# Kernel optimization log

Hardware: AMD Instinct MI355X
Metric: run time of the kernel (lower is better)

The kernel has to match this reference:

```python
import jax, jax.numpy as jnp
import numpy as np

B, T, E, H, K, V = 256, 200, 100, 128, 13, 50000


def run_lstm(x, W, U, b, reverse=False):
    """Keras LSTM with activation=relu, recurrent_activation=sigmoid.
    x: [B,T,E]; W: [E,4H]; U: [H,4H]; b: [4H]. Gate order: i, f, g, o.
    Returns hidden states [B,T,H] (time-aligned for both directions)."""
    Bn = x.shape[0]
    Hn = U.shape[0]
    xw = jnp.einsum('bte,eg->btg', x, W) + b  # precompute input projections [B,T,4H]

    def step(carry, xw_t):
        h, c = carry
        z = xw_t + h @ U
        i, f, g, o = jnp.split(z, 4, axis=-1)
        i = jax.nn.sigmoid(i)
        f = jax.nn.sigmoid(f)
        g = jax.nn.relu(g)          # activation=relu (non-cuDNN path in TF)
        c = f * c + i * g
        h = o * jax.nn.relu(c)      # output activation also relu
        return (h, c), h

    init = (jnp.zeros((Bn, Hn), x.dtype), jnp.zeros((Bn, Hn), x.dtype))
    _, hs = jax.lax.scan(step, init, jnp.swapaxes(xw, 0, 1), reverse=reverse)
    return jnp.swapaxes(hs, 0, 1)


def crf_log_likelihood(logits, labels, lens, trans):
    """tfa.text.crf_log_likelihood: score(labels) - logZ, masked by seq lens."""
    Bn, Tn, Kn = logits.shape
    t_idx = jnp.arange(Tn)
    mask = t_idx[None, :] < lens[:, None]  # [B,T]
    # unary score
    unary = jnp.take_along_axis(logits, labels[..., None], axis=-1)[..., 0]
    u_score = jnp.sum(jnp.where(mask, unary, 0.0), axis=-1)
    # transition score
    pair = trans[labels[:, :-1], labels[:, 1:]]  # [B,T-1]
    pmask = t_idx[None, 1:] < lens[:, None]
    b_score = jnp.sum(jnp.where(pmask, pair, 0.0), axis=-1)
    # forward algorithm (log-space DP over time, masked updates)
    def step(alpha, inp):
        logit_t, valid = inp  # [B,K], [B]
        new = jax.nn.logsumexp(alpha[:, :, None] + trans[None], axis=1) + logit_t
        alpha = jnp.where(valid[:, None], new, alpha)
        return alpha, None

    alpha0 = logits[:, 0, :]
    xs = (jnp.swapaxes(logits[:, 1:, :], 0, 1), jnp.swapaxes(mask[:, 1:], 0, 1))
    alpha, _ = jax.lax.scan(step, alpha0, xs)
    logZ = jax.nn.logsumexp(alpha, axis=-1)
    return u_score + b_score - logZ


def setup_inputs() -> dict:
    key = jax.random.key(0)
    ks = jax.random.split(key, 12)
    s = lambda k, shape, sc: jax.random.normal(k, shape, jnp.float32) * sc
    return {
        'text': jax.random.randint(ks[0], (B, T), 0, V).astype(jnp.int32),
        'labels': jax.random.randint(ks[1], (B, T), 0, K).astype(jnp.int32),
        'emb': s(ks[2], (V, E), 0.1),
        'Wf': s(ks[3], (E, 4 * H), 0.05),
        'Uf': s(ks[4], (H, 4 * H), 0.05),
        'bf': jnp.zeros((4 * H,), jnp.float32),
        'Wb': s(ks[5], (E, 4 * H), 0.05),
        'Ub': s(ks[6], (H, 4 * H), 0.05),
        'bb': jnp.zeros((4 * H,), jnp.float32),
        'Wd': s(ks[7], (2 * H, K), 0.05),
        'bd': jnp.zeros((K,), jnp.float32),
        'trans': jax.random.uniform(ks[8], (K, K), jnp.float32),
    }


def reference(text, labels, emb, Wf, Uf, bf, Wb, Ub, bb, Wd, bd, trans):
    lens = jnp.sum((text != 0).astype(jnp.int32), axis=-1)  # [B]
    x = emb[text]                      # embedding lookup [B,T,E]
    # dropout is identity in eval mode
    h_fwd = run_lstm(x, Wf, Uf, bf, reverse=False)
    h_bwd = run_lstm(x, Wb, Ub, bb, reverse=True)
    h = jnp.concatenate([h_fwd, h_bwd], axis=-1)  # [B,T,2H]
    logits = jax.nn.softmax(h @ Wd + bd, axis=-1)  # Dense(softmax), per source
    log_likelihood = crf_log_likelihood(logits, labels, lens, trans)
    return logits, lens, log_likelihood
```

## Files before the change

kernel.cpp:

```cpp
#include <hip/hip_runtime.h>
#include <hip/hip_bf16.h>

#define Bn 256
#define Tn 200
#define En 100
#define Hn 128
#define Kn 13
#define G4 512
#define BT 51200

typedef __attribute__((ext_vector_type(8))) __bf16 bf8_t;
typedef __attribute__((ext_vector_type(4))) unsigned short us4_t;
typedef __attribute__((ext_vector_type(4))) float f4_t;

__device__ __forceinline__ unsigned short f2bf(float f) {
  unsigned int u = __float_as_uint(f);
  u = (u + 0x7FFFu + ((u >> 16) & 1u)) >> 16;
  return (unsigned short)u;
}
__device__ __forceinline__ float bf2f(unsigned short s) {
  return __uint_as_float(((unsigned int)s) << 16);
}
__device__ __forceinline__ float sigm(float x) { return 1.f / (1.f + __expf(-x)); }

__device__ __forceinline__ void bar_lgkm() {
  asm volatile("s_waitcnt lgkmcnt(0)" ::: "memory");
  __builtin_amdgcn_s_barrier();
  __builtin_amdgcn_sched_barrier(0);
}

__device__ __forceinline__ int gperm(int n) {
  return ((n >> 4) & 3) * 128 + ((n >> 6) << 4) + (n & 15);
}

__global__ __launch_bounds__(64) void k_lens(const int* __restrict__ text,
                                             int* __restrict__ lens_i,
                                             float* __restrict__ out_lens) {
  int b = blockIdx.x, lane = threadIdx.x;
  int cnt = 0;
  for (int t = lane; t < Tn; t += 64) cnt += (text[b * Tn + t] != 0);
  for (int off = 32; off; off >>= 1) cnt += __shfl_down(cnt, off);
  if (lane == 0) { lens_i[b] = cnt; out_lens[b] = (float)cnt; }
}

__global__ __launch_bounds__(256) void k_wt(const float* __restrict__ Wf,
                                            const float* __restrict__ Wb,
                                            const float* __restrict__ Uf,
                                            const float* __restrict__ Ub,
                                            unsigned short* __restrict__ wt,
                                            unsigned short* __restrict__ ut) {
  int idx = blockIdx.x * 256 + threadIdx.x;
  int half = idx >> 17;
  int rem = idx & 131071;
  int dir = rem >> 16;
  int nk = rem & 65535;
  int n = nk >> 7, k = nk & 127;
  int mc = gperm(n);
  if (half == 0) {
    const float* W = dir ? Wb : Wf;
    wt[rem] = f2bf((k < En) ? W[k * G4 + mc] : 0.f);
  } else {
    const float* U = dir ? Ub : Uf;
    ut[rem] = f2bf(U[k * G4 + mc]);
  }
}

__global__ __launch_bounds__(256) void k_gather(const int* __restrict__ text,
                                                const float* __restrict__ emb,
                                                unsigned short* __restrict__ xg) {
  int row = blockIdx.x * 128 + (threadIdx.x >> 1);
  int half = threadIdx.x & 1;
  int tok = text[row];
  const float* er = emb + (size_t)tok * En;
  unsigned short* xr = xg + (size_t)row * 128 + half * 64;
  #pragma unroll
  for (int c = 0; c < 64; c += 2) {
    int col = half * 64 + c;
    float v0 = (col < En) ? er[col] : 0.f;
    float v1 = (col + 1 < En) ? er[col + 1] : 0.f;
    unsigned int pk = (unsigned int)f2bf(v0) | ((unsigned int)f2bf(v1) << 16);
    *(unsigned int*)(xr + c) = pk;
  }
}

__global__ __launch_bounds__(256) void k_gemm_xw(const unsigned short* __restrict__ xg,
                                                 const unsigned short* __restrict__ wt,
                                                 const float* __restrict__ biasf,
                                                 const float* __restrict__ biasb,
                                                 unsigned short* __restrict__ xwf,
                                                 unsigned short* __restrict__ xwb) {
  __shared__ unsigned short As[128 * 128];
  __shared__ unsigned short Bs[128 * 128];
  int mt = blockIdx.x;
  int dir = blockIdx.y >> 2;
  int nt = blockIdx.y & 3;
  const float* bias = dir ? biasb : biasf;
  unsigned short* out = dir ? xwb : xwf;
  int tid = threadIdx.x;
  const unsigned short* wt_d = wt + (size_t)dir * (G4 * 128);

  #pragma unroll
  for (int it = 0; it < 8; it++) {
    int idx = it * 256 + tid;
    int r = idx >> 4, c = idx & 15;
    bf8_t va = *(const bf8_t*)(xg + ((size_t)mt * 128 + r) * 128 + c * 8);
    bf8_t vb = *(const bf8_t*)(wt_d + ((size_t)nt * 128 + r) * 128 + c * 8);
    int byte = (r * 256 + c * 16) ^ ((r & 7) << 4);
    *(bf8_t*)((char*)As + byte) = va;
    *(bf8_t*)((char*)Bs + byte) = vb;
  }
  __syncthreads();
  int wid = tid >> 6, lane = tid & 63;
  int wm = wid >> 1, wn = wid & 1;
  int lr = lane & 15, lk = lane >> 4;
  f4_t zero = {0.f, 0.f, 0.f, 0.f};
  f4_t acc[4][4];
  #pragma unroll
  for (int m = 0; m < 4; m++)
    #pragma unroll
    for (int n = 0; n < 4; n++) acc[m][n] = zero;
  #pragma unroll
  for (int kk = 0; kk < 4; kk++) {
    bf8_t af[4], bv[4];
    #pragma unroll
    for (int m = 0; m < 4; m++) {
      int r = wm * 64 + m * 16 + lr;
      int byte = (r * 256 + kk * 64 + lk * 16) ^ ((r & 7) << 4);
      af[m] = *(const bf8_t*)((const char*)As + byte);
    }
    #pragma unroll
    for (int n = 0; n < 4; n++) {
      int r = wn * 64 + n * 16 + lr;
      int byte = (r * 256 + kk * 64 + lk * 16) ^ ((r & 7) << 4);
      bv[n] = *(const bf8_t*)((const char*)Bs + byte);
    }
    #pragma unroll
    for (int m = 0; m < 4; m++)
      #pragma unroll
      for (int n = 0; n < 4; n++)
        acc[m][n] = __builtin_amdgcn_mfma_f32_16x16x32_bf16(af[m], bv[n], acc[m][n], 0, 0, 0);
  }
  float bn[4];
  #pragma unroll
  for (int n = 0; n < 4; n++) {
    int colg = nt * 128 + wn * 64 + n * 16 + lr;
    bn[n] = bias[gperm(colg)];
  }
  int w2 = nt * 2 + wn;
  #pragma unroll
  for (int m = 0; m < 4; m++) {
    int rowl = wm * 64 + m * 16 + lk * 4;
    #pragma unroll
    for (int q = 0; q < 4; q++) {
      int row = mt * 128 + rowl + q;
      int b = row / 200;
      int t = row - b * 200;
      int bg = b >> 2, lg2 = b & 3;
      int tid2 = w2 * 64 + lg2 * 16 + lr;
      size_t dst = (((size_t)t * 64 + bg) * 512 + tid2) * 4;
      us4_t v;
      v[0] = f2bf(acc[m][0][q] + bn[0]);
      v[1] = f2bf(acc[m][1][q] + bn[1]);
      v[2] = f2bf(acc[m][2][q] + bn[2]);
      v[3] = f2bf(acc[m][3][q] + bn[3]);
      *(us4_t*)(out + dst) = v;
    }
  }
}

#define UB16(M) M(0,0) M(0,1) M(0,2) M(0,3) M(1,0) M(1,1) M(1,2) M(1,3) \
                M(2,0) M(2,1) M(2,2) M(2,3) M(3,0) M(3,1) M(3,2) M(3,3)

__global__ __attribute__((amdgpu_flat_work_group_size(512, 512),
                          amdgpu_waves_per_eu(1, 2)))
void k_scan(const unsigned short* __restrict__ ut,
            const unsigned short* __restrict__ xw2,
            unsigned short* __restrict__ hf,
            unsigned short* __restrict__ hb) {
  int blk = blockIdx.x;
  int dir = blk >> 6;
  int bg = blk & 63;
  int b0 = bg * 4;
  int tid = threadIdx.x;
  int w = tid >> 6, l = tid & 63;
  int lr = l & 15, lg = l >> 4;
  int jj = w * 16 + lr;
  const unsigned short* ut_d = ut + (size_t)dir * (G4 * 128);
  const unsigned short* xw_d = xw2 + (size_t)dir * ((size_t)BT * G4);
  unsigned short* hout = dir ? hb : hf;
  int t0 = dir ? (Tn - 1) : 0;
  int dt = dir ? -1 : 1;

#define LOADUB(nt, kk) \
  bf8_t ub_##nt##_##kk = *(const bf8_t*)(ut_d + (size_t)(w * 64 + (nt) * 16 + lr) * 128 + (kk) * 32 + lg * 8); \
  asm volatile("" : "+a"(ub_##nt##_##kk));
  UB16(LOADUB)
#undef LOADUB

  __shared__ unsigned short h_lds[2][2048];
  for (int i = tid; i < 2048; i += 512) ((unsigned int*)h_lds)[i] = 0;

  int rb0 = (lr * 256 +   0 + lg * 16) ^ ((lr & 7) << 4);
  int rb1 = (lr * 256 +  64 + lg * 16) ^ ((lr & 7) << 4);
  int rb2 = (lr * 256 + 128 + lg * 16) ^ ((lr & 7) << 4);
  int rb3 = (lr * 256 + 192 + lg * 16) ^ ((lr & 7) << 4);
  int wb = (((lg * 4) * 256 + jj * 2) ^ (((lg * 4) & 7) << 4)) + 4096;
  char* lbase = (char*)h_lds;

  const unsigned short* xptr = xw_d + (((size_t)t0 * 64 + bg) * 512 + tid) * 4;
  const long long xstep = (long long)dt * 131072;
  unsigned short* hp = hout + ((size_t)t0 * Bn + b0 + lg) * 128 + jj;
  const long long hstep = (long long)dt * Bn * 128;

  us4_t xa = *(const us4_t*)(xptr);
  us4_t xb = *(const us4_t*)(xptr + xstep);
  xptr += 2 * xstep;

  float c0 = 0.f;
  f4_t acc0 = {0.f,0.f,0.f,0.f}, acc1 = {0.f,0.f,0.f,0.f};
  f4_t acc2 = {0.f,0.f,0.f,0.f}, acc3 = {0.f,0.f,0.f,0.f};
  bar_lgkm();

#define MF(nt, kk) acc##nt = __builtin_amdgcn_mfma_f32_16x16x32_bf16(af##kk, ub_##nt##_##kk, acc##nt, 0, 0, 0);
#define STEP(X, ISSUE_OK) { \
    acc0[0] = bf2f(X[0]); acc1[0] = bf2f(X[1]); \
    acc2[0] = bf2f(X[2]); acc3[0] = bf2f(X[3]); \
    if (ISSUE_OK) { X = *(const us4_t*)(xptr); } \
    xptr += xstep; \
    bf8_t af0 = *(const bf8_t*)(lbase + rb0); \
    bf8_t af1 = *(const bf8_t*)(lbase + rb1); \
    bf8_t af2 = *(const bf8_t*)(lbase + rb2); \
    bf8_t af3 = *(const bf8_t*)(lbase + rb3); \
    MF(0,0) MF(1,0) MF(2,0) MF(3,0) \
    MF(0,1) MF(1,1) MF(2,1) MF(3,1) \
    MF(0,2) MF(1,2) MF(2,2) MF(3,2) \
    MF(0,3) MF(1,3) MF(2,3) MF(3,3) \
    float ig = sigm(acc0[0]); \
    float fg = sigm(acc1[0]); \
    float gg = fmaxf(acc2[0], 0.f); \
    c0 = fmaf(fg, c0, ig * gg); \
    unsigned short hs2 = f2bf(sigm(acc3[0]) * fmaxf(c0, 0.f)); \
    *(unsigned short*)(lbase + wb) = hs2; \
    bar_lgkm(); \
    hp[0] = hs2; \
    rb0 ^= 4096; rb1 ^= 4096; rb2 ^= 4096; rb3 ^= 4096; wb ^= 4096; \
    hp += hstep; }

  for (int tt = 0; tt < Tn; tt += 2) {
    STEP(xa, tt < Tn - 2)
    STEP(xb, tt < Tn - 3)
  }
#undef STEP
#undef MF
}

__global__ __launch_bounds__(128) void k_logits(const unsigned short* __restrict__ hf,
                                                const unsigned short* __restrict__ hb,
                                                const float* __restrict__ Wd,
                                                const float* __restrict__ bd,
                                                float* __restrict__ out) {
  __shared__ unsigned short hs[128 * 256];
  int tid = threadIdx.x;
  size_t row0 = (size_t)blockIdx.x * 128;
  #pragma unroll
  for (int it = 0; it < 16; it++) {
    int idx = it * 128 + tid;
    int r = idx >> 4, c = idx & 15;
    bf8_t vf = *(const bf8_t*)(hf + (row0 + r) * 128 + c * 8);
    bf8_t vb = *(const bf8_t*)(hb + (row0 + r) * 128 + c * 8);
    int byte = (r * 512 + c * 16) ^ ((r & 7) << 4);
    *(bf8_t*)((char*)hs + byte) = vf;
    int byte2 = (r * 512 + 256 + c * 16) ^ ((r & 7) << 4);
    *(bf8_t*)((char*)hs + byte2) = vb;
  }
  __syncthreads();
  float acc[Kn];
  #pragma unroll
  for (int jj = 0; jj < Kn; jj++) acc[jj] = bd[jj];
  int r = tid;
  #pragma unroll 4
  for (int c = 0; c < 32; c++) {
    int byte = (r * 512 + c * 16) ^ ((r & 7) << 4);
    bf8_t v = *(const bf8_t*)((const char*)hs + byte);
    #pragma unroll
    for (int e = 0; e < 8; e++) {
      float h = (float)v[e];
      int k = c * 8 + e;
      #pragma unroll
      for (int jj = 0; jj < Kn; jj++)
        acc[jj] = fmaf(h, Wd[k * Kn + jj], acc[jj]);
    }
  }
  float m = acc[0];
  #pragma unroll
  for (int jj = 1; jj < Kn; jj++) m = fmaxf(m, acc[jj]);
  float s = 0.f;
  #pragma unroll
  for (int jj = 0; jj < Kn; jj++) { acc[jj] = __expf(acc[jj] - m); s += acc[jj]; }
  float inv = 1.f / s;
  int rg = (int)row0 + tid;
  int b = rg & 255, t = rg >> 8;
  float* op = out + ((size_t)b * Tn + t) * Kn;
  #pragma unroll
  for (int jj = 0; jj < Kn; jj++) op[jj] = acc[jj] * inv;
}

__global__ __launch_bounds__(64) void k_crf(const float* __restrict__ logits,
                                            const int* __restrict__ labels,
                                            const int* __restrict__ lens_i,
                                            const float* __restrict__ trans,
                                            float* __restrict__ out_ll) {
  int b = blockIdx.x, lane = threadIdx.x;
  int len = lens_i[b];
  const float* lg = logits + (size_t)b * Tn * Kn;
  const int* lab = labels + (size_t)b * Tn;
  float sc = 0.f;
  for (int t = lane; t < Tn; t += 64) {
    if (t < len) {
      sc += lg[t * Kn + lab[t]];
      if (t >= 1) sc += trans[lab[t - 1] * Kn + lab[t]];
    }
  }
  for (int off = 32; off; off >>= 1) sc += __shfl_down(sc, off);
  bool act = lane < Kn;
  int jl = act ? lane : 0;
  float etr[Kn];
  #pragma unroll
  for (int i = 0; i < Kn; i++) etr[i] = __expf(trans[i * Kn + jl]);
  float a = act ? lg[jl] : -INFINITY;
  float lgv = (len > 1) ? lg[Kn + jl] : 0.f;
  for (int t = 1; t < len; t++) {
    float lgn = (t + 1 < len) ? lg[(t + 1) * Kn + jl] : 0.f;
    float m = a;
    for (int off = 8; off; off >>= 1) m = fmaxf(m, __shfl_xor(m, off, 16));
    float ea = __expf(a - m);
    float s = 0.f;
    #pragma unroll
    for (int i = 0; i < Kn; i++) s = fmaf(__shfl(ea, i), etr[i], s);
    float anew = m + __logf(s) + lgv;
    if (act) a = anew;
    lgv = lgn;
  }
  float m2 = a;
  for (int off = 8; off; off >>= 1) m2 = fmaxf(m2, __shfl_xor(m2, off, 16));
  float ea2 = act ? __expf(a - m2) : 0.f;
  float ssum = ea2;
  for (int off = 8; off; off >>= 1) ssum += __shfl_xor(ssum, off, 16);
  float logZ = m2 + __logf(ssum);
  if (lane == 0) out_ll[b] = sc - logZ;
}

extern "C" void kernel_launch(void* const* d_in, const int* in_sizes, int n_in,
                              void* d_out, int out_size, void* d_ws, size_t ws_size,
                              hipStream_t stream) {
  const int* text = (const int*)d_in[0];
  const int* labels = (const int*)d_in[1];
  const float* emb = (const float*)d_in[2];
  const float* Wf = (const float*)d_in[3];
  const float* Uf = (const float*)d_in[4];
  const float* bf_ = (const float*)d_in[5];
  const float* Wb = (const float*)d_in[6];
  const float* Ub = (const float*)d_in[7];
  const float* bb_ = (const float*)d_in[8];
  const float* Wd = (const float*)d_in[9];
  const float* bd = (const float*)d_in[10];
  const float* trans = (const float*)d_in[11];
  (void)in_sizes; (void)n_in; (void)out_size; (void)ws_size;

  float* out = (float*)d_out;
  float* out_logits = out;
  float* out_lens = out + (size_t)BT * Kn;
  float* out_ll = out_lens + Bn;

  char* ws = (char*)d_ws;
  size_t o = 0;
  int* lens_i = (int*)(ws + o);                o += 1024;
  unsigned short* wt = (unsigned short*)(ws + o);  o += (size_t)2 * G4 * 128 * 2;
  unsigned short* ut = (unsigned short*)(ws + o);  o += (size_t)2 * G4 * 128 * 2;
  unsigned short* xg = (unsigned short*)(ws + o);  o += (size_t)BT * 128 * 2;
  unsigned short* xw_s = (unsigned short*)(ws + o); o += (size_t)2 * BT * G4 * 2;
  unsigned short* hfb = (unsigned short*)(ws + o); o += (size_t)BT * Hn * 2;
  unsigned short* hbb = (unsigned short*)(ws + o); o += (size_t)BT * Hn * 2;
  unsigned short* xwf = xw_s;
  unsigned short* xwb = xw_s + (size_t)BT * G4;

  hipLaunchKernelGGL(k_lens, dim3(Bn), dim3(64), 0, stream, text, lens_i, out_lens);
  hipLaunchKernelGGL(k_wt, dim3(1024), dim3(256), 0, stream, Wf, Wb, Uf, Ub, wt, ut);
  hipLaunchKernelGGL(k_gather, dim3(400), dim3(256), 0, stream, text, emb, xg);
  hipLaunchKernelGGL(k_gemm_xw, dim3(400, 8), dim3(256), 0, stream, xg, wt, bf_, bb_, xwf, xwb);
  hipLaunchKernelGGL(k_scan, dim3(128), dim3(512), 0, stream, ut, xw_s, hfb, hbb);
  hipLaunchKernelGGL(k_logits, dim3(400), dim3(128), 0, stream, hfb, hbb, Wd, bd, out_logits);
  hipLaunchKernelGGL(k_crf, dim3(Bn), dim3(64), 0, stream, out_logits, labels, lens_i, trans, out_ll);
}
```

Measured before the change: 297.7 us.

## Fuse embedding gather into input GEMM and merge small prep kernels

Folds the embedding gather into the input-projection GEMM. Each 512-thread block now gathers 64 token rows straight into swizzled LDS, loads its slice of the weight matrix directly into registers, and covers all 512 gate columns. This removes the intermediate xg buffer and its round trip through memory. The lens and weight-transpose kernels become a single k_prep launch, which cuts launch overhead. The scan loop now issues its LDS loads before the x-projection prefetch and makes that prefetch unconditional. As a result it reads a little past the end of each direction's xw buffer, staying inside the workspace, in exchange for simpler scheduling.

```diff
diff --git a/kernel.cpp b/kernel.cpp
--- a/kernel.cpp
+++ b/kernel.cpp
@@ -33,130 +33,143 @@
   return ((n >> 4) & 3) * 128 + ((n >> 6) << 4) + (n & 15);
 }
 
-__global__ __launch_bounds__(64) void k_lens(const int* __restrict__ text,
-                                             int* __restrict__ lens_i,
-                                             float* __restrict__ out_lens) {
-  int b = blockIdx.x, lane = threadIdx.x;
-  int cnt = 0;
-  for (int t = lane; t < Tn; t += 64) cnt += (text[b * Tn + t] != 0);
-  for (int off = 32; off; off >>= 1) cnt += __shfl_down(cnt, off);
-  if (lane == 0) { lens_i[b] = cnt; out_lens[b] = (float)cnt; }
-}
-
-__global__ __launch_bounds__(256) void k_wt(const float* __restrict__ Wf,
-                                            const float* __restrict__ Wb,
-                                            const float* __restrict__ Uf,
-                                            const float* __restrict__ Ub,
-                                            unsigned short* __restrict__ wt,
-                                            unsigned short* __restrict__ ut) {
-  int idx = blockIdx.x * 256 + threadIdx.x;
-  int half = idx >> 17;
-  int rem = idx & 131071;
-  int dir = rem >> 16;
-  int nk = rem & 65535;
-  int n = nk >> 7, k = nk & 127;
-  int mc = gperm(n);
-  if (half == 0) {
-    const float* W = dir ? Wb : Wf;
-    wt[rem] = f2bf((k < En) ? W[k * G4 + mc] : 0.f);
+__global__ __launch_bounds__(256) void k_prep(const int* __restrict__ text,
+                                              const float* __restrict__ Wf,
+                                              const float* __restrict__ Wb,
+                                              const float* __restrict__ Uf,
+                                              const float* __restrict__ Ub,
+                                              unsigned short* __restrict__ wt,
+                                              unsigned short* __restrict__ ut,
+                                              int* __restrict__ lens_i,
+                                              float* __restrict__ out_lens) {
+  int bx = blockIdx.x;
+  if (bx < 1024) {
+    int idx = bx * 256 + threadIdx.x;
+    int half = idx >> 17;
+    int rem = idx & 131071;
+    int dir = rem >> 16;
+    int nk = rem & 65535;
+    int n = nk >> 7, k = nk & 127;
+    int mc = gperm(n);
+    if (half == 0) {
+      const float* W = dir ? Wb : Wf;
+      wt[rem] = f2bf((k < En) ? W[k * G4 + mc] : 0.f);
+    } else {
+      const float* U = dir ? Ub : Uf;
+      ut[rem] = f2bf(U[k * G4 + mc]);
+    }
   } else {
-    const float* U = dir ? Ub : Uf;
-    ut[rem] = f2bf(U[k * G4 + mc]);
-  }
-}
-
-__global__ __launch_bounds__(256) void k_gather(const int* __restrict__ text,
-                                                const float* __restrict__ emb,
-                                                unsigned short* __restrict__ xg) {
-  int row = blockIdx.x * 128 + (threadIdx.x >> 1);
-  int half = threadIdx.x & 1;
-  int tok = text[row];
-  const float* er = emb + (size_t)tok * En;
-  unsigned short* xr = xg + (size_t)row * 128 + half * 64;
-  #pragma unroll
-  for (int c = 0; c < 64; c += 2) {
-    int col = half * 64 + c;
-    float v0 = (col < En) ? er[col] : 0.f;
-    float v1 = (col + 1 < En) ? er[col + 1] : 0.f;
-    unsigned int pk = (unsigned int)f2bf(v0) | ((unsigned int)f2bf(v1) << 16);
-    *(unsigned int*)(xr + c) = pk;
-  }
-}
-
-__global__ __launch_bounds__(256) void k_gemm_xw(const unsigned short* __restrict__ xg,
+    int wi = threadIdx.x >> 6, lane = threadIdx.x & 63;
+    int b = (bx - 1024) * 4 + wi;
+    int cnt = 0;
+    for (int t = lane; t < Tn; t += 64) cnt += (text[b * Tn + t] != 0);
+    for (int off = 32; off; off >>= 1) cnt += __shfl_down(cnt, off);
+    if (lane == 0) { lens_i[b] = cnt; out_lens[b] = (float)cnt; }
+  }
+}
+
+#define NB16(M) M(0,0) M(0,1) M(0,2) M(0,3) M(1,0) M(1,1) M(1,2) M(1,3) \
+                M(2,0) M(2,1) M(2,2) M(2,3) M(3,0) M(3,1) M(3,2) M(3,3)
+
+__global__ __launch_bounds__(512) void k_gemm_xw(const int* __restrict__ text,
+                                                 const float* __restrict__ emb,
                                                  const unsigned short* __restrict__ wt,
                                                  const float* __restrict__ biasf,
                                                  const float* __restrict__ biasb,
                                                  unsigned short* __restrict__ xwf,
                                                  unsigned short* __restrict__ xwb) {
-  __shared__ unsigned short As[128 * 128];
-  __shared__ unsigned short Bs[128 * 128];
-  int mt = blockIdx.x;
-  int dir = blockIdx.y >> 2;
-  int nt = blockIdx.y & 3;
+  __shared__ unsigned short As[64 * 128];
+  int bx = blockIdx.x;
+  int dir = (bx >= 800);
+  int mt = dir ? bx - 800 : bx;
   const float* bias = dir ? biasb : biasf;
   unsigned short* out = dir ? xwb : xwf;
   int tid = threadIdx.x;
   const unsigned short* wt_d = wt + (size_t)dir * (G4 * 128);
 
-  #pragma unroll
-  for (int it = 0; it < 8; it++) {
-    int idx = it * 256 + tid;
-    int r = idx >> 4, c = idx & 15;
-    bf8_t va = *(const bf8_t*)(xg + ((size_t)mt * 128 + r) * 128 + c * 8);
-    bf8_t vb = *(const bf8_t*)(wt_d + ((size_t)nt * 128 + r) * 128 + c * 8);
-    int byte = (r * 256 + c * 16) ^ ((r & 7) << 4);
-    *(bf8_t*)((char*)As + byte) = va;
-    *(bf8_t*)((char*)Bs + byte) = vb;
-  }
+  {
+    int row = tid >> 3;
+    int oct = tid & 7;
+    int tok = text[mt * 64 + row];
+    const float* er = emb + (size_t)tok * En;
+    float fv[16];
+    #pragma unroll
+    for (int i = 0; i < 16; i++) fv[i] = 0.f;
+    if (oct < 6) {
+      #pragma unroll
+      for (int i = 0; i < 4; i++) {
+        float4 v = *(const float4*)(er + oct * 16 + i * 4);
+        fv[i * 4 + 0] = v.x; fv[i * 4 + 1] = v.y; fv[i * 4 + 2] = v.z; fv[i * 4 + 3] = v.w;
+      }
+    } else if (oct == 6) {
+      float4 v = *(const float4*)(er + 96);
+      fv[0] = v.x; fv[1] = v.y; fv[2] = v.z; fv[3] = v.w;
+    }
+    int swz = (row & 7) << 4;
+    #pragma unroll
+    for (int j = 0; j < 2; j++) {
+      unsigned short pk[8];
+      #pragma unroll
+      for (int e = 0; e < 8; e++) pk[e] = f2bf(fv[j * 8 + e]);
+      int byte = (row * 256 + oct * 32 + j * 16) ^ swz;
+      *(bf8_t*)((char*)As + byte) = *(bf8_t*)pk;
+    }
+  }
+
+  int w = tid >> 6, l = tid & 63;
+  int lr = l & 15, lg = l >> 4, lk = lg;
+#define LOADB(n, kk) \
+  bf8_t bb_##n##_##kk = *(const bf8_t*)(wt_d + (size_t)(w * 64 + (n) * 16 + lr) * 128 + (kk) * 32 + lg * 8);
+  NB16(LOADB)
+#undef LOADB
   __syncthreads();
-  int wid = tid >> 6, lane = tid & 63;
-  int wm = wid >> 1, wn = wid & 1;
-  int lr = lane & 15, lk = lane >> 4;
+
   f4_t zero = {0.f, 0.f, 0.f, 0.f};
   f4_t acc[4][4];
   #pragma unroll
   for (int m = 0; m < 4; m++)
     #pragma unroll
     for (int n = 0; n < 4; n++) acc[m][n] = zero;
-  #pragma unroll
-  for (int kk = 0; kk < 4; kk++) {
-    bf8_t af[4], bv[4];
-    #pragma unroll
-    for (int m = 0; m < 4; m++) {
-      int r = wm * 64 + m * 16 + lr;
-      int byte = (r * 256 + kk * 64 + lk * 16) ^ ((r & 7) << 4);
-      af[m] = *(const bf8_t*)((const char*)As + byte);
-    }
-    #pragma unroll
-    for (int n = 0; n < 4; n++) {
-      int r = wn * 64 + n * 16 + lr;
-      int byte = (r * 256 + kk * 64 + lk * 16) ^ ((r & 7) << 4);
-      bv[n] = *(const bf8_t*)((const char*)Bs + byte);
-    }
-    #pragma unroll
-    for (int m = 0; m < 4; m++)
-      #pragma unroll
-      for (int n = 0; n < 4; n++)
-        acc[m][n] = __builtin_amdgcn_mfma_f32_16x16x32_bf16(af[m], bv[n], acc[m][n], 0, 0, 0);
-  }
+
+  const char* lAs = (const char*)As;
+  int sz = (lr & 7) << 4;
+#define MFK(kk) { \
+    bf8_t a0 = *(const bf8_t*)(lAs + (((0 * 16 + lr) * 256 + (kk) * 64 + lg * 16) ^ sz)); \
+    bf8_t a1 = *(const bf8_t*)(lAs + (((1 * 16 + lr) * 256 + (kk) * 64 + lg * 16) ^ sz)); \
+    bf8_t a2 = *(const bf8_t*)(lAs + (((2 * 16 + lr) * 256 + (kk) * 64 + lg * 16) ^ sz)); \
+    bf8_t a3 = *(const bf8_t*)(lAs + (((3 * 16 + lr) * 256 + (kk) * 64 + lg * 16) ^ sz)); \
+    acc[0][0] = __builtin_amdgcn_mfma_f32_16x16x32_bf16(a0, bb_0_##kk, acc[0][0], 0, 0, 0); \
+    acc[0][1] = __builtin_amdgcn_mfma_f32_16x16x32_bf16(a0, bb_1_##kk, acc[0][1], 0, 0, 0); \
+    acc[0][2] = __builtin_amdgcn_mfma_f32_16x16x32_bf16(a0, bb_2_##kk, acc[0][2], 0, 0, 0); \
+    acc[0][3] = __builtin_amdgcn_mfma_f32_16x16x32_bf16(a0, bb_3_##kk, acc[0][3], 0, 0, 0); \
+    acc[1][0] = __builtin_amdgcn_mfma_f32_16x16x32_bf16(a1, bb_0_##kk, acc[1][0], 0, 0, 0); \
+    acc[1][1] = __builtin_amdgcn_mfma_f32_16x16x32_bf16(a1, bb_1_##kk, acc[1][1], 0, 0, 0); \
+    acc[1][2] = __builtin_amdgcn_mfma_f32_16x16x32_bf16(a1, bb_2_##kk, acc[1][2], 0, 0, 0); \
+    acc[1][3] = __builtin_amdgcn_mfma_f32_16x16x32_bf16(a1, bb_3_##kk, acc[1][3], 0, 0, 0); \
+    acc[2][0] = __builtin_amdgcn_mfma_f32_16x16x32_bf16(a2, bb_0_##kk, acc[2][0], 0, 0, 0); \
+    acc[2][1] = __builtin_amdgcn_mfma_f32_16x16x32_bf16(a2, bb_1_##kk, acc[2][1], 0, 0, 0); \
+    acc[2][2] = __builtin_amdgcn_mfma_f32_16x16x32_bf16(a2, bb_2_##kk, acc[2][2], 0, 0, 0); \
+    acc[2][3] = __builtin_amdgcn_mfma_f32_16x16x32_bf16(a2, bb_3_##kk, acc[2][3], 0, 0, 0); \
+    acc[3][0] = __builtin_amdgcn_mfma_f32_16x16x32_bf16(a3, bb_0_##kk, acc[3][0], 0, 0, 0); \
+    acc[3][1] = __builtin_amdgcn_mfma_f32_16x16x32_bf16(a3, bb_1_##kk, acc[3][1], 0, 0, 0); \
+    acc[3][2] = __builtin_amdgcn_mfma_f32_16x16x32_bf16(a3, bb_2_##kk, acc[3][2], 0, 0, 0); \
+    acc[3][3] = __builtin_amdgcn_mfma_f32_16x16x32_bf16(a3, bb_3_##kk, acc[3][3], 0, 0, 0); }
+  MFK(0) MFK(1) MFK(2) MFK(3)
+#undef MFK
+
   float bn[4];
   #pragma unroll
-  for (int n = 0; n < 4; n++) {
-    int colg = nt * 128 + wn * 64 + n * 16 + lr;
-    bn[n] = bias[gperm(colg)];
-  }
-  int w2 = nt * 2 + wn;
+  for (int n = 0; n < 4; n++) bn[n] = bias[gperm(w * 64 + n * 16 + lr)];
   #pragma unroll
   for (int m = 0; m < 4; m++) {
-    int rowl = wm * 64 + m * 16 + lk * 4;
+    int rowl = m * 16 + lk * 4;
     #pragma unroll
     for (int q = 0; q < 4; q++) {
-      int row = mt * 128 + rowl + q;
+      int row = mt * 64 + rowl + q;
       int b = row / 200;
       int t = row - b * 200;
       int bg = b >> 2, lg2 = b & 3;
-      int tid2 = w2 * 64 + lg2 * 16 + lr;
+      int tid2 = w * 64 + lg2 * 16 + lr;
       size_t dst = (((size_t)t * 64 + bg) * 512 + tid2) * 4;
       us4_t v;
       v[0] = f2bf(acc[m][0][q] + bn[0]);
@@ -222,15 +235,15 @@
   bar_lgkm();
 
 #define MF(nt, kk) acc##nt = __builtin_amdgcn_mfma_f32_16x16x32_bf16(af##kk, ub_##nt##_##kk, acc##nt, 0, 0, 0);
-#define STEP(X, ISSUE_OK) { \
-    acc0[0] = bf2f(X[0]); acc1[0] = bf2f(X[1]); \
-    acc2[0] = bf2f(X[2]); acc3[0] = bf2f(X[3]); \
-    if (ISSUE_OK) { X = *(const us4_t*)(xptr); } \
-    xptr += xstep; \
+#define STEP(X) { \
     bf8_t af0 = *(const bf8_t*)(lbase + rb0); \
     bf8_t af1 = *(const bf8_t*)(lbase + rb1); \
     bf8_t af2 = *(const bf8_t*)(lbase + rb2); \
     bf8_t af3 = *(const bf8_t*)(lbase + rb3); \
+    acc0[0] = bf2f(X[0]); acc1[0] = bf2f(X[1]); \
+    acc2[0] = bf2f(X[2]); acc3[0] = bf2f(X[3]); \
+    X = *(const us4_t*)(xptr);     \
+    xptr += xstep; \
     MF(0,0) MF(1,0) MF(2,0) MF(3,0) \
     MF(0,1) MF(1,1) MF(2,1) MF(3,1) \
     MF(0,2) MF(1,2) MF(2,2) MF(3,2) \
@@ -247,8 +260,8 @@
     hp += hstep; }
 
   for (int tt = 0; tt < Tn; tt += 2) {
-    STEP(xa, tt < Tn - 2)
-    STEP(xb, tt < Tn - 3)
+    STEP(xa)
+    STEP(xb)
   }
 #undef STEP
 #undef MF
@@ -377,17 +390,16 @@
   int* lens_i = (int*)(ws + o);                o += 1024;
   unsigned short* wt = (unsigned short*)(ws + o);  o += (size_t)2 * G4 * 128 * 2;
   unsigned short* ut = (unsigned short*)(ws + o);  o += (size_t)2 * G4 * 128 * 2;
-  unsigned short* xg = (unsigned short*)(ws + o);  o += (size_t)BT * 128 * 2;
   unsigned short* xw_s = (unsigned short*)(ws + o); o += (size_t)2 * BT * G4 * 2;
   unsigned short* hfb = (unsigned short*)(ws + o); o += (size_t)BT * Hn * 2;
   unsigned short* hbb = (unsigned short*)(ws + o); o += (size_t)BT * Hn * 2;
   unsigned short* xwf = xw_s;
   unsigned short* xwb = xw_s + (size_t)BT * G4;
 
-  hipLaunchKernelGGL(k_lens, dim3(Bn), dim3(64), 0, stream, text, lens_i, out_lens);
-  hipLaunchKernelGGL(k_wt, dim3(1024), dim3(256), 0, stream, Wf, Wb, Uf, Ub, wt, ut);
-  hipLaunchKernelGGL(k_gather, dim3(400), dim3(256), 0, stream, text, emb, xg);
-  hipLaunchKernelGGL(k_gemm_xw, dim3(400, 8), dim3(256), 0, stream, xg, wt, bf_, bb_, xwf, xwb);
+  hipLaunchKernelGGL(k_prep, dim3(1088), dim3(256), 0, stream,
+                     text, Wf, Wb, Uf, Ub, wt, ut, lens_i, out_lens);
+  hipLaunchKernelGGL(k_gemm_xw, dim3(1600), dim3(512), 0, stream,
+                     text, emb, wt, bf_, bb_, xwf, xwb);
   hipLaunchKernelGGL(k_scan, dim3(128), dim3(512), 0, stream, ut, xw_s, hfb, hbb);
   hipLaunchKernelGGL(k_logits, dim3(400), dim3(128), 0, stream, hfb, hbb, Wd, bd, out_logits);
   hipLaunchKernelGGL(k_crf, dim3(Bn), dim3(64), 0, stream, out_logits, labels, lens_i, trans, out_ll);
```

Result: faster. 288.9 us (-3.0%).
